# Kernel tuning notes

Measured on AMD Instinct MI355X. Metric: run time of the kernel, lower is better.

The kernel has to match this reference:

```python
import jax, jax.numpy as jnp
import numpy as np

N_NODES = 50000
N_EDGES = 25000
NNZ = 600000
D = 128
H = 256
DEPTH = 2


def setup_inputs() -> dict:
    key = jax.random.key(0)
    ks = jax.random.split(key, 12)
    x = jax.random.normal(ks[0], (N_NODES, D), dtype=jnp.float32)
    v_idx = jax.random.randint(ks[1], (NNZ,), 0, N_NODES)
    e_idx = jax.random.randint(ks[2], (NNZ,), 0, N_EDGES)
    s = 0.05
    W1 = jax.random.normal(ks[3], (H, D), dtype=jnp.float32) * s
    b1 = jnp.zeros((H,), jnp.float32)
    W2 = jax.random.normal(ks[4], (D, H), dtype=jnp.float32) * s
    b2 = jnp.zeros((D,), jnp.float32)
    Wu = jax.random.normal(ks[5], (D, D), dtype=jnp.float32) * s
    bu = jnp.zeros((D,), jnp.float32)
    Wa = jax.random.normal(ks[6], (4, D), dtype=jnp.float32) * s
    ba = jnp.zeros((4,), jnp.float32)
    return {"x": x, "v_idx": v_idx, "e_idx": e_idx, "W1": W1, "b1": b1,
            "W2": W2, "b2": b2, "Wu": Wu, "bu": bu, "Wa": Wa, "ba": ba}


def reference(x, v_idx, e_idx, W1, b1, W2, b2, Wu, bu, Wa, ba):
    ones = jnp.ones((v_idx.shape[0],), x.dtype)
    # degrees for mean aggregation (clamped to avoid div-by-zero)
    edeg = jnp.maximum(jax.ops.segment_sum(ones, e_idx, num_segments=N_EDGES), 1.0)
    vdeg = jnp.maximum(jax.ops.segment_sum(ones, v_idx, num_segments=N_NODES), 1.0)

    def v2v_mean(m):
        # vertex -> hyperedge (mean), then hyperedge -> vertex (mean)
        e_feat = jax.ops.segment_sum(m[v_idx], e_idx, num_segments=N_EDGES) / edeg[:, None]
        return jax.ops.segment_sum(e_feat[e_idx], v_idx, num_segments=N_NODES) / vdeg[:, None]

    def update(h):
        m = jax.nn.relu(h @ W1.T + b1)   # [N, H]
        m = jax.nn.relu(m @ W2.T + b2)   # [N, D]  (dropout = identity in eval)
        m_i = v2v_mean(m)                # [N, D]
        return jax.nn.relu(h @ Wu.T + bu + m_i)

    for _ in range(DEPTH):
        x = update(x)
    a = x @ Wa.T + ba                    # [N, 4]
    return jax.nn.log_softmax(a, axis=1)
```

## Files before the change

### kernel.cpp

```cpp
#include <hip/hip_runtime.h>
#include <hip/hip_bf16.h>
#include <math.h>

#define N_NODES 50000
#define N_EDGES 25000
#define NNZ     600000
#define D       128
#define H       256

#define BW    98
#define NBE   256
#define NBV   511
#define CAPE  3072
#define CAPV  1536
#define CHUNK 4096

typedef short short8 __attribute__((ext_vector_type(8)));
typedef float floatx4 __attribute__((ext_vector_type(4)));

__device__ inline ushort f2bf(float f) {
    uint u = __float_as_uint(f);
    u += 0x7FFF + ((u >> 16) & 1);
    return (ushort)(u >> 16);
}
__device__ inline float bflo(uint u) { return __uint_as_float(u << 16); }
__device__ inline float bfhi(uint u) { return __uint_as_float(u & 0xffff0000u); }

__global__ void convert_and_place(const float* __restrict__ W1, ushort* __restrict__ W1b,
                                  const float* __restrict__ W2, ushort* __restrict__ W2b,
                                  const float* __restrict__ Wu, ushort* __restrict__ Wub,
                                  const int* __restrict__ v_idx, const int* __restrict__ e_idx,
                                  int* __restrict__ cntE, int* __restrict__ cntV,
                                  int2* __restrict__ recE, int2* __restrict__ recV,
                                  int convBlocks) {
    if ((int)blockIdx.x < convBlocks) {
        const int n1 = H * D / 4;
        const int n2 = D * H / 4;
        const int nu = D * D / 4;
        int j = blockIdx.x * 256 + threadIdx.x;
        const float* src; ushort* dst;
        if (j < n1)                { src = W1; dst = W1b; }
        else if ((j -= n1) < n2)   { src = W2; dst = W2b; }
        else if ((j -= n2) < nu)   { src = Wu; dst = Wub; }
        else return;
        float4 v = ((const float4*)src)[j];
        ushort4 o;
        o.x = f2bf(v.x); o.y = f2bf(v.y); o.z = f2bf(v.z); o.w = f2bf(v.w);
        ((ushort4*)dst)[j] = o;
        return;
    }

    __shared__ int hE[NBE], hV[NBV];
    __shared__ int rE[NBE], rV[NBV];
    for (int i = threadIdx.x; i < NBE; i += 256) hE[i] = 0;
    for (int i = threadIdx.x; i < NBV; i += 256) hV[i] = 0;
    __syncthreads();
    int base = (blockIdx.x - convBlocks) * CHUNK;
    int end  = min(base + CHUNK, NNZ);
    int myE[16], myV[16];
    #pragma unroll
    for (int j = 0; j < 16; ++j) {
        int i = base + threadIdx.x + j * 256;
        myE[j] = -1; myV[j] = -1;
        if (i < end) {
            myE[j] = e_idx[i];
            myV[j] = v_idx[i];
            atomicAdd(&hE[myE[j] / BW], 1);
            atomicAdd(&hV[myV[j] / BW], 1);
        }
    }
    __syncthreads();
    for (int i = threadIdx.x; i < NBE; i += 256) {
        int c = hE[i];
        rE[i] = c ? atomicAdd(&cntE[i], c) : 0;
    }
    for (int i = threadIdx.x; i < NBV; i += 256) {
        int c = hV[i];
        rV[i] = c ? atomicAdd(&cntV[i], c) : 0;
    }
    __syncthreads();
    for (int i = threadIdx.x; i < NBE; i += 256) hE[i] = 0;
    for (int i = threadIdx.x; i < NBV; i += 256) hV[i] = 0;
    __syncthreads();
    #pragma unroll
    for (int j = 0; j < 16; ++j) {
        if (myE[j] >= 0) {
            int bk = myE[j] / BW;
            int p = rE[bk] + atomicAdd(&hE[bk], 1);
            recE[(size_t)bk * CAPE + p] = make_int2(myE[j], myV[j]);
            bk = myV[j] / BW;
            p = rV[bk] + atomicAdd(&hV[bk], 1);
            recV[(size_t)bk * CAPV + p] = make_int2(myV[j], myE[j]);
        }
    }
}

__global__ void bucket_final(const int2* __restrict__ recE, const int* __restrict__ cntE,
                             const int2* __restrict__ recV, const int* __restrict__ cntV,
                             int2* __restrict__ e_sd, float* __restrict__ erecip, int* __restrict__ e_vert,
                             int2* __restrict__ v_sd, float* __restrict__ vrecip, int* __restrict__ v_edge) {
    __shared__ int hist[BW], scn[BW], cur[BW];
    const bool eSide = blockIdx.x < NBE;
    const int b = eSide ? blockIdx.x : blockIdx.x - NBE;
    const int cap   = eSide ? CAPE : CAPV;
    const int2* rec = (eSide ? recE : recV) + (size_t)b * cap;
    const int cnt   = (eSide ? cntE : cntV)[b];
    const int nseg  = eSide ? N_EDGES : N_NODES;
    int2* sd        = eSide ? e_sd : v_sd;
    float* recip    = eSide ? erecip : vrecip;
    int* outv       = (eSide ? e_vert : v_edge) + (size_t)b * cap;
    const int k0 = b * BW;

    for (int i = threadIdx.x; i < BW; i += 256) hist[i] = 0;
    __syncthreads();
    for (int i = threadIdx.x; i < cnt; i += 256)
        atomicAdd(&hist[rec[i].x - k0], 1);
    __syncthreads();

    if (threadIdx.x < 64) {
        int lane = threadIdx.x;
        int v0 = hist[lane];
        int a = v0;
        #pragma unroll
        for (int d = 1; d < 64; d <<= 1) {
            int u = __shfl_up(a, d, 64);
            if (lane >= d) a += u;
        }
        scn[lane] = a - v0;
        int tot0 = __shfl(a, 63, 64);
        int v1 = (lane < BW - 64) ? hist[64 + lane] : 0;
        int a1 = v1;
        #pragma unroll
        for (int d = 1; d < 64; d <<= 1) {
            int u = __shfl_up(a1, d, 64);
            if (lane >= d) a1 += u;
        }
        if (lane < BW - 64) scn[64 + lane] = tot0 + a1 - v1;
    }
    __syncthreads();

    const int gbase = b * cap;
    for (int i = threadIdx.x; i < BW; i += 256) {
        int seg = k0 + i;
        if (seg < nseg) {
            sd[seg] = make_int2(gbase + scn[i], hist[i]);
            recip[seg] = 1.0f / (float)max(hist[i], 1);
        }
        cur[i] = scn[i];
    }
    __syncthreads();
    for (int i = threadIdx.x; i < cnt; i += 256) {
        int2 r = rec[i];
        int p = atomicAdd(&cur[r.x - k0], 1);
        outv[p] = r.y;
    }
}

__global__ void gather_rows(const ushort* __restrict__ src,
                            const int2* __restrict__ sd,
                            const int* __restrict__ list,
                            const float* __restrict__ recip,
                            const ushort* __restrict__ uadd,
                            ushort* __restrict__ outbuf,
                            const float* __restrict__ Wa,
                            const float* __restrict__ ba,
                            float* __restrict__ headout,
                            int nseg) {
    long long gtid = (long long)blockIdx.x * blockDim.x + threadIdx.x;
    int seg = (int)(gtid >> 4);
    int ql  = threadIdx.x & 15;
    if (seg >= nseg) return;
    int2 dsc = sd[seg];
    int s = dsc.x, cnt = dsc.y;
    const ushort* sp = src + ql * 8;

    float f0 = 0.f, f1 = 0.f, f2 = 0.f, f3 = 0.f;
    float f4 = 0.f, f5 = 0.f, f6 = 0.f, f7 = 0.f;

    int p = 0;
    for (; p + 4 <= cnt; p += 4) {
        int r0 = list[s + p + 0];
        int r1 = list[s + p + 1];
        int r2 = list[s + p + 2];
        int r3 = list[s + p + 3];
        uint4 t0 = *(const uint4*)(sp + (size_t)r0 * D);
        uint4 t1 = *(const uint4*)(sp + (size_t)r1 * D);
        uint4 t2 = *(const uint4*)(sp + (size_t)r2 * D);
        uint4 t3 = *(const uint4*)(sp + (size_t)r3 * D);
        f0 += bflo(t0.x) + bflo(t1.x) + bflo(t2.x) + bflo(t3.x);
        f1 += bfhi(t0.x) + bfhi(t1.x) + bfhi(t2.x) + bfhi(t3.x);
        f2 += bflo(t0.y) + bflo(t1.y) + bflo(t2.y) + bflo(t3.y);
        f3 += bfhi(t0.y) + bfhi(t1.y) + bfhi(t2.y) + bfhi(t3.y);
        f4 += bflo(t0.z) + bflo(t1.z) + bflo(t2.z) + bflo(t3.z);
        f5 += bfhi(t0.z) + bfhi(t1.z) + bfhi(t2.z) + bfhi(t3.z);
        f6 += bflo(t0.w) + bflo(t1.w) + bflo(t2.w) + bflo(t3.w);
        f7 += bfhi(t0.w) + bfhi(t1.w) + bfhi(t2.w) + bfhi(t3.w);
    }
    for (; p < cnt; ++p) {
        int r0 = list[s + p];
        uint4 t0 = *(const uint4*)(sp + (size_t)r0 * D);
        f0 += bflo(t0.x);  f1 += bfhi(t0.x);
        f2 += bflo(t0.y);  f3 += bfhi(t0.y);
        f4 += bflo(t0.z);  f5 += bfhi(t0.z);
        f6 += bflo(t0.w);  f7 += bfhi(t0.w);
    }

    float rc = recip[seg];
    f0 *= rc; f1 *= rc; f2 *= rc; f3 *= rc;
    f4 *= rc; f5 *= rc; f6 *= rc; f7 *= rc;
    if (uadd) {
        uint4 uv = *(const uint4*)(uadd + (size_t)seg * D + ql * 8);
        f0 = fmaxf(f0 + bflo(uv.x), 0.f);  f1 = fmaxf(f1 + bfhi(uv.x), 0.f);
        f2 = fmaxf(f2 + bflo(uv.y), 0.f);  f3 = fmaxf(f3 + bfhi(uv.y), 0.f);
        f4 = fmaxf(f4 + bflo(uv.z), 0.f);  f5 = fmaxf(f5 + bfhi(uv.z), 0.f);
        f6 = fmaxf(f6 + bflo(uv.w), 0.f);  f7 = fmaxf(f7 + bfhi(uv.w), 0.f);
    }
    if (headout) {
        float av[4];
        #pragma unroll
        for (int j = 0; j < 4; ++j) {
            const float* wr = Wa + j * D + ql * 8;
            float4 wA = *(const float4*)wr;
            float4 wB = *(const float4*)(wr + 4);
            float pj = f0 * wA.x + f1 * wA.y + f2 * wA.z + f3 * wA.w
                     + f4 * wB.x + f5 * wB.y + f6 * wB.z + f7 * wB.w;
            pj += __shfl_xor(pj, 1, 64);
            pj += __shfl_xor(pj, 2, 64);
            pj += __shfl_xor(pj, 4, 64);
            pj += __shfl_xor(pj, 8, 64);
            av[j] = pj + ba[j];
        }
        if (ql == 0) {
            float mx = fmaxf(fmaxf(av[0], av[1]), fmaxf(av[2], av[3]));
            float se = expf(av[0] - mx) + expf(av[1] - mx)
                     + expf(av[2] - mx) + expf(av[3] - mx);
            float lse = mx + logf(se);
            float4 o = make_float4(av[0] - lse, av[1] - lse, av[2] - lse, av[3] - lse);
            *(float4*)(headout + (size_t)seg * 4) = o;
        }
    } else {
        uint4 o;
        o.x = ((uint)f2bf(f1) << 16) | (uint)f2bf(f0);
        o.y = ((uint)f2bf(f3) << 16) | (uint)f2bf(f2);
        o.z = ((uint)f2bf(f5) << 16) | (uint)f2bf(f4);
        o.w = ((uint)f2bf(f7) << 16) | (uint)f2bf(f6);
        *(uint4*)(outbuf + (size_t)seg * D + ql * 8) = o;
    }
}

__launch_bounds__(256, 2)
__global__ void mlp_fused(const void* __restrict__ Aptr, int a_fp32,
                          const ushort* __restrict__ W1b,
                          const float* __restrict__ b1,
                          const ushort* __restrict__ W2b,
                          const float* __restrict__ b2,
                          const ushort* __restrict__ Wub,
                          const float* __restrict__ bu,
                          ushort* __restrict__ m2out,
                          ushort* __restrict__ uout,
                          int M) {
    __shared__ ushort Af[128][136];
    __shared__ __align__(16) char Pbuf[18432];
    __shared__ ushort m1c[128][72];
    ushort* P = (ushort*)Pbuf;

    const int tid = threadIdx.x;
    const int w = tid >> 6, lane = tid & 63;
    const int quad = lane >> 4, mrow = lane & 15;
    const int rowBase = blockIdx.x * 128;

    #pragma unroll
    for (int r = 0; r < 8; ++r) {
        int idx = tid + r * 256;
        int row = idx >> 4;
        int c   = (idx & 15) << 3;
        uint4 av = make_uint4(0, 0, 0, 0);
        if (rowBase + row < M) {
            if (a_fp32) {
                const float* ap = (const float*)Aptr + (size_t)(rowBase + row) * D + c;
                float4 va = *(const float4*)ap;
                float4 vb = *(const float4*)(ap + 4);
                av.x = ((uint)f2bf(va.y) << 16) | (uint)f2bf(va.x);
                av.y = ((uint)f2bf(va.w) << 16) | (uint)f2bf(va.z);
                av.z = ((uint)f2bf(vb.y) << 16) | (uint)f2bf(vb.x);
                av.w = ((uint)f2bf(vb.w) << 16) | (uint)f2bf(vb.z);
            } else {
                av = *(const uint4*)((const ushort*)Aptr + (size_t)(rowBase + row) * D + c);
            }
        }
        *(uint4*)&Af[row][c] = av;
    }

    for (int n0 = 0; n0 < D; n0 += 64) {
        __syncthreads();
        #pragma unroll
        for (int r = 0; r < 4; ++r) {
            int idx = tid + r * 256;
            int row = idx >> 4;
            int c   = (idx & 15) << 3;
            *(uint4*)&P[row * 136 + c] = *(const uint4*)(Wub + (size_t)(n0 + row) * D + c);
        }
        __syncthreads();
        #pragma unroll
        for (int rg = 0; rg < 2; ++rg) {
            floatx4 acc[4] = {{0,0,0,0},{0,0,0,0},{0,0,0,0},{0,0,0,0}};
            #pragma unroll
            for (int k0 = 0; k0 < D; k0 += 32) {
                short8 af = *(const short8*)&Af[rg * 64 + w * 16 + mrow][k0 + quad * 8];
                #pragma unroll
                for (int t = 0; t < 4; ++t) {
                    short8 bfr = *(const short8*)&P[(t * 16 + mrow) * 136 + k0 + quad * 8];
                    acc[t] = __builtin_amdgcn_mfma_f32_16x16x32_bf16(af, bfr, acc[t], 0, 0, 0);
                }
            }
            int growb = rowBase + rg * 64 + w * 16 + quad * 4;
            if (growb < M) {
                #pragma unroll
                for (int t = 0; t < 4; ++t) {
                    float bb = bu[n0 + t * 16 + mrow];
                    #pragma unroll
                    for (int r = 0; r < 4; ++r)
                        uout[(size_t)(growb + r) * D + n0 + t * 16 + mrow] =
                            f2bf(acc[t][r] + bb);
                }
            }
        }
    }

    floatx4 acc2[2][8] = {};
    for (int kc = 0; kc < 4; ++kc) {
        __syncthreads();
        #pragma unroll
        for (int r = 0; r < 4; ++r) {
            int idx = tid + r * 256;
            int row = idx >> 4;
            int c   = (idx & 15) << 3;
            *(uint4*)&P[row * 136 + c] = *(const uint4*)(W1b + (size_t)(kc * 64 + row) * D + c);
        }
        __syncthreads();
        #pragma unroll
        for (int rg = 0; rg < 2; ++rg) {
            floatx4 acc1[4] = {{0,0,0,0},{0,0,0,0},{0,0,0,0},{0,0,0,0}};
            #pragma unroll
            for (int k0 = 0; k0 < D; k0 += 32) {
                short8 af = *(const short8*)&Af[rg * 64 + w * 16 + mrow][k0 + quad * 8];
                #pragma unroll
                for (int t = 0; t < 4; ++t) {
                    short8 bfr = *(const short8*)&P[(t * 16 + mrow) * 136 + k0 + quad * 8];
                    acc1[t] = __builtin_amdgcn_mfma_f32_16x16x32_bf16(af, bfr, acc1[t], 0, 0, 0);
                }
            }
            #pragma unroll
            for (int t = 0; t < 4; ++t) {
                float bb = b1[kc * 64 + t * 16 + mrow];
                #pragma unroll
                for (int r = 0; r < 4; ++r)
                    m1c[rg * 64 + w * 16 + quad * 4 + r][t * 16 + mrow] =
                        f2bf(fmaxf(acc1[t][r] + bb, 0.f));
            }
        }
        __syncthreads();
        #pragma unroll
        for (int r = 0; r < 4; ++r) {
            int idx = tid + r * 256;
            int row = idx >> 3;
            int c8  = (idx & 7) << 3;
            *(uint4*)&P[row * 72 + c8] = *(const uint4*)(W2b + (size_t)row * H + kc * 64 + c8);
        }
        __syncthreads();
        #pragma unroll
        for (int rg = 0; rg < 2; ++rg) {
            #pragma unroll
            for (int k0 = 0; k0 < 64; k0 += 32) {
                short8 af = *(const short8*)&m1c[rg * 64 + w * 16 + mrow][k0 + quad * 8];
                #pragma unroll
                for (int t2 = 0; t2 < 8; ++t2) {
                    short8 bfr = *(const short8*)&P[(t2 * 16 + mrow) * 72 + k0 + quad * 8];
                    acc2[rg][t2] = __builtin_amdgcn_mfma_f32_16x16x32_bf16(af, bfr, acc2[rg][t2], 0, 0, 0);
                }
            }
        }
    }

    #pragma unroll
    for (int rg = 0; rg < 2; ++rg) {
        int growb = rowBase + rg * 64 + w * 16 + quad * 4;
        if (growb < M) {
            #pragma unroll
            for (int t2 = 0; t2 < 8; ++t2) {
                float bb = b2[t2 * 16 + mrow];
                #pragma unroll
                for (int r = 0; r < 4; ++r)
                    m2out[(size_t)(growb + r) * D + t2 * 16 + mrow] =
                        f2bf(fmaxf(acc2[rg][t2][r] + bb, 0.f));
            }
        }
    }
}

extern "C" void kernel_launch(void* const* d_in, const int* in_sizes, int n_in,
                              void* d_out, int out_size, void* d_ws, size_t ws_size,
                              hipStream_t stream) {
    const float* x     = (const float*)d_in[0];
    const int*   v_idx = (const int*)d_in[1];
    const int*   e_idx = (const int*)d_in[2];
    const float* W1    = (const float*)d_in[3];
    const float* b1    = (const float*)d_in[4];
    const float* W2    = (const float*)d_in[5];
    const float* b2    = (const float*)d_in[6];
    const float* Wu    = (const float*)d_in[7];
    const float* bu    = (const float*)d_in[8];
    const float* Wa    = (const float*)d_in[9];
    const float* ba    = (const float*)d_in[10];
    float* out = (float*)d_out;

    char* wsp = (char*)d_ws;
    auto alloc = [&](size_t bytes) -> char* {
        char* p = wsp;
        wsp += (bytes + 255) & ~(size_t)255;
        return p;
    };

    ushort* hA     = (ushort*)alloc((size_t)N_NODES * D * 2);
    ushort* m2b    = (ushort*)alloc((size_t)N_NODES * D * 2);
    ushort* ub     = (ushort*)alloc((size_t)N_NODES * D * 2);
    ushort* e_feat = (ushort*)alloc((size_t)N_EDGES * D * 2);
    ushort* W1b    = (ushort*)alloc((size_t)H * D * 2);
    ushort* W2b    = (ushort*)alloc((size_t)D * H * 2);
    ushort* Wub    = (ushort*)alloc((size_t)D * D * 2);
    int*    e_vert = (int*)alloc((size_t)NBE * CAPE * 4);
    int*    v_edge = (int*)alloc((size_t)NBV * CAPV * 4);
    int2*   recE   = (int2*)alloc((size_t)NBE * CAPE * 8);
    int2*   recV   = (int2*)alloc((size_t)NBV * CAPV * 8);
    int*    cntE   = (int*)alloc((size_t)(NBE + NBV) * 4);
    int*    cntV   = cntE + NBE;
    int2*   e_sd   = (int2*)alloc((size_t)N_EDGES * 8);
    int2*   v_sd   = (int2*)alloc((size_t)N_NODES * 8);
    float*  erecip = (float*)alloc((size_t)N_EDGES * 4);
    float*  vrecip = (float*)alloc((size_t)N_NODES * 4);

    const int cooBlocks  = (NNZ + CHUNK - 1) / CHUNK;
    const int convTotal  = H * D / 4 + D * H / 4 + D * D / 4;
    const int convBlocks = (convTotal + 255) / 256;

    hipMemsetAsync(cntE, 0, (size_t)(NBE + NBV) * 4, stream);
    convert_and_place<<<convBlocks + cooBlocks, 256, 0, stream>>>(
        W1, W1b, W2, W2b, Wu, Wub, v_idx, e_idx, cntE, cntV, recE, recV, convBlocks);
    bucket_final<<<NBE + NBV, 256, 0, stream>>>(recE, cntE, recV, cntV,
                                                e_sd, erecip, e_vert,
                                                v_sd, vrecip, v_edge);

    const int gridM = (N_NODES + 127) / 128;
    const int gEdge = (N_EDGES * 16 + 255) / 256;
    const int gVert = (N_NODES * 16 + 255) / 256;

    const void* h = x;
    int h_fp32 = 1;
    for (int depth = 0; depth < 2; ++depth) {
        mlp_fused<<<gridM, 256, 0, stream>>>(h, h_fp32, W1b, b1, W2b, b2, Wub, bu,
                                             m2b, ub, N_NODES);
        gather_rows<<<gEdge, 256, 0, stream>>>(
            m2b, e_sd, e_vert, erecip, nullptr, e_feat, nullptr, nullptr, nullptr, N_EDGES);
        if (depth == 0) {
            gather_rows<<<gVert, 256, 0, stream>>>(
                e_feat, v_sd, v_edge, vrecip, ub, hA, nullptr, nullptr, nullptr, N_NODES);
            h = hA;
            h_fp32 = 0;
        } else {
            gather_rows<<<gVert, 256, 0, stream>>>(
                e_feat, v_sd, v_edge, vrecip, ub, nullptr, Wa, ba, out, N_NODES);
        }
    }
}
```

Before: 253.4 us.

## Use 512-thread MLP blocks with one row-group per wave; unroll gather by 8

```diff
diff --git a/kernel.cpp b/kernel.cpp
--- a/kernel.cpp
+++ b/kernel.cpp
@@ -178,6 +178,40 @@
     float f4 = 0.f, f5 = 0.f, f6 = 0.f, f7 = 0.f;
 
     int p = 0;
+    for (; p + 8 <= cnt; p += 8) {
+        int r0 = list[s + p + 0];
+        int r1 = list[s + p + 1];
+        int r2 = list[s + p + 2];
+        int r3 = list[s + p + 3];
+        int r4 = list[s + p + 4];
+        int r5 = list[s + p + 5];
+        int r6 = list[s + p + 6];
+        int r7 = list[s + p + 7];
+        uint4 t0 = *(const uint4*)(sp + (size_t)r0 * D);
+        uint4 t1 = *(const uint4*)(sp + (size_t)r1 * D);
+        uint4 t2 = *(const uint4*)(sp + (size_t)r2 * D);
+        uint4 t3 = *(const uint4*)(sp + (size_t)r3 * D);
+        uint4 t4 = *(const uint4*)(sp + (size_t)r4 * D);
+        uint4 t5 = *(const uint4*)(sp + (size_t)r5 * D);
+        uint4 t6 = *(const uint4*)(sp + (size_t)r6 * D);
+        uint4 t7 = *(const uint4*)(sp + (size_t)r7 * D);
+        f0 += bflo(t0.x)+bflo(t1.x)+bflo(t2.x)+bflo(t3.x)
+            + bflo(t4.x)+bflo(t5.x)+bflo(t6.x)+bflo(t7.x);
+        f1 += bfhi(t0.x)+bfhi(t1.x)+bfhi(t2.x)+bfhi(t3.x)
+            + bfhi(t4.x)+bfhi(t5.x)+bfhi(t6.x)+bfhi(t7.x);
+        f2 += bflo(t0.y)+bflo(t1.y)+bflo(t2.y)+bflo(t3.y)
+            + bflo(t4.y)+bflo(t5.y)+bflo(t6.y)+bflo(t7.y);
+        f3 += bfhi(t0.y)+bfhi(t1.y)+bfhi(t2.y)+bfhi(t3.y)
+            + bfhi(t4.y)+bfhi(t5.y)+bfhi(t6.y)+bfhi(t7.y);
+        f4 += bflo(t0.z)+bflo(t1.z)+bflo(t2.z)+bflo(t3.z)
+            + bflo(t4.z)+bflo(t5.z)+bflo(t6.z)+bflo(t7.z);
+        f5 += bfhi(t0.z)+bfhi(t1.z)+bfhi(t2.z)+bfhi(t3.z)
+            + bfhi(t4.z)+bfhi(t5.z)+bfhi(t6.z)+bfhi(t7.z);
+        f6 += bflo(t0.w)+bflo(t1.w)+bflo(t2.w)+bflo(t3.w)
+            + bflo(t4.w)+bflo(t5.w)+bflo(t6.w)+bflo(t7.w);
+        f7 += bfhi(t0.w)+bfhi(t1.w)+bfhi(t2.w)+bfhi(t3.w)
+            + bfhi(t4.w)+bfhi(t5.w)+bfhi(t6.w)+bfhi(t7.w);
+    }
     for (; p + 4 <= cnt; p += 4) {
         int r0 = list[s + p + 0];
         int r1 = list[s + p + 1];
@@ -248,7 +282,7 @@
     }
 }
 
-__launch_bounds__(256, 2)
+__launch_bounds__(512, 4)
 __global__ void mlp_fused(const void* __restrict__ Aptr, int a_fp32,
                           const ushort* __restrict__ W1b,
                           const float* __restrict__ b1,
@@ -265,13 +299,15 @@
     ushort* P = (ushort*)Pbuf;
 
     const int tid = threadIdx.x;
-    const int w = tid >> 6, lane = tid & 63;
+    const int w = tid >> 6;
+    const int lane = tid & 63;
     const int quad = lane >> 4, mrow = lane & 15;
     const int rowBase = blockIdx.x * 128;
+    const int wr0 = w * 16;
 
     #pragma unroll
-    for (int r = 0; r < 8; ++r) {
-        int idx = tid + r * 256;
+    for (int r = 0; r < 4; ++r) {
+        int idx = tid + r * 512;
         int row = idx >> 4;
         int c   = (idx & 15) << 3;
         uint4 av = make_uint4(0, 0, 0, 0);
@@ -294,97 +330,87 @@
     for (int n0 = 0; n0 < D; n0 += 64) {
         __syncthreads();
         #pragma unroll
-        for (int r = 0; r < 4; ++r) {
-            int idx = tid + r * 256;
+        for (int r = 0; r < 2; ++r) {
+            int idx = tid + r * 512;
             int row = idx >> 4;
             int c   = (idx & 15) << 3;
             *(uint4*)&P[row * 136 + c] = *(const uint4*)(Wub + (size_t)(n0 + row) * D + c);
         }
         __syncthreads();
-        #pragma unroll
-        for (int rg = 0; rg < 2; ++rg) {
-            floatx4 acc[4] = {{0,0,0,0},{0,0,0,0},{0,0,0,0},{0,0,0,0}};
+        floatx4 acc[4] = {{0,0,0,0},{0,0,0,0},{0,0,0,0},{0,0,0,0}};
+        #pragma unroll
+        for (int k0 = 0; k0 < D; k0 += 32) {
+            short8 af = *(const short8*)&Af[wr0 + mrow][k0 + quad * 8];
             #pragma unroll
-            for (int k0 = 0; k0 < D; k0 += 32) {
-                short8 af = *(const short8*)&Af[rg * 64 + w * 16 + mrow][k0 + quad * 8];
+            for (int t = 0; t < 4; ++t) {
+                short8 bfr = *(const short8*)&P[(t * 16 + mrow) * 136 + k0 + quad * 8];
+                acc[t] = __builtin_amdgcn_mfma_f32_16x16x32_bf16(af, bfr, acc[t], 0, 0, 0);
+            }
+        }
+        int growb = rowBase + wr0 + quad * 4;
+        if (growb < M) {
+            #pragma unroll
+            for (int t = 0; t < 4; ++t) {
+                float bb = bu[n0 + t * 16 + mrow];
                 #pragma unroll
-                for (int t = 0; t < 4; ++t) {
-                    short8 bfr = *(const short8*)&P[(t * 16 + mrow) * 136 + k0 + quad * 8];
-                    acc[t] = __builtin_amdgcn_mfma_f32_16x16x32_bf16(af, bfr, acc[t], 0, 0, 0);
-                }
+                for (int r = 0; r < 4; ++r)
+                    uout[(size_t)(growb + r) * D + n0 + t * 16 + mrow] =
+                        f2bf(acc[t][r] + bb);
             }
-            int growb = rowBase + rg * 64 + w * 16 + quad * 4;
-            if (growb < M) {
-                #pragma unroll
-                for (int t = 0; t < 4; ++t) {
-                    float bb = bu[n0 + t * 16 + mrow];
-                    #pragma unroll
-                    for (int r = 0; r < 4; ++r)
-                        uout[(size_t)(growb + r) * D + n0 + t * 16 + mrow] =
-                            f2bf(acc[t][r] + bb);
-                }
-            }
-        }
-    }
-
-    floatx4 acc2[2][8] = {};
+        }
+    }
+
+    floatx4 acc2[8] = {};
     for (int kc = 0; kc < 4; ++kc) {
         __syncthreads();
         #pragma unroll
-        for (int r = 0; r < 4; ++r) {
-            int idx = tid + r * 256;
+        for (int r = 0; r < 2; ++r) {
+            int idx = tid + r * 512;
             int row = idx >> 4;
             int c   = (idx & 15) << 3;
             *(uint4*)&P[row * 136 + c] = *(const uint4*)(W1b + (size_t)(kc * 64 + row) * D + c);
         }
         __syncthreads();
-        #pragma unroll
-        for (int rg = 0; rg < 2; ++rg) {
-            floatx4 acc1[4] = {{0,0,0,0},{0,0,0,0},{0,0,0,0},{0,0,0,0}};
-            #pragma unroll
-            for (int k0 = 0; k0 < D; k0 += 32) {
-                short8 af = *(const short8*)&Af[rg * 64 + w * 16 + mrow][k0 + quad * 8];
-                #pragma unroll
-                for (int t = 0; t < 4; ++t) {
-                    short8 bfr = *(const short8*)&P[(t * 16 + mrow) * 136 + k0 + quad * 8];
-                    acc1[t] = __builtin_amdgcn_mfma_f32_16x16x32_bf16(af, bfr, acc1[t], 0, 0, 0);
-                }
-            }
+        floatx4 acc1[4] = {{0,0,0,0},{0,0,0,0},{0,0,0,0},{0,0,0,0}};
+        #pragma unroll
+        for (int k0 = 0; k0 < D; k0 += 32) {
+            short8 af = *(const short8*)&Af[wr0 + mrow][k0 + quad * 8];
             #pragma unroll
             for (int t = 0; t < 4; ++t) {
-                float bb = b1[kc * 64 + t * 16 + mrow];
-                #pragma unroll
-                for (int r = 0; r < 4; ++r)
-                    m1c[rg * 64 + w * 16 + quad * 4 + r][t * 16 + mrow] =
-                        f2bf(fmaxf(acc1[t][r] + bb, 0.f));
+                short8 bfr = *(const short8*)&P[(t * 16 + mrow) * 136 + k0 + quad * 8];
+                acc1[t] = __builtin_amdgcn_mfma_f32_16x16x32_bf16(af, bfr, acc1[t], 0, 0, 0);
             }
         }
+        #pragma unroll
+        for (int t = 0; t < 4; ++t) {
+            float bb = b1[kc * 64 + t * 16 + mrow];
+            #pragma unroll
+            for (int r = 0; r < 4; ++r)
+                m1c[wr0 + quad * 4 + r][t * 16 + mrow] =
+                    f2bf(fmaxf(acc1[t][r] + bb, 0.f));
+        }
         __syncthreads();
         #pragma unroll
-        for (int r = 0; r < 4; ++r) {
-            int idx = tid + r * 256;
+        for (int r = 0; r < 2; ++r) {
+            int idx = tid + r * 512;
             int row = idx >> 3;
             int c8  = (idx & 7) << 3;
             *(uint4*)&P[row * 72 + c8] = *(const uint4*)(W2b + (size_t)row * H + kc * 64 + c8);
         }
         __syncthreads();
         #pragma unroll
-        for (int rg = 0; rg < 2; ++rg) {
+        for (int k0 = 0; k0 < 64; k0 += 32) {
+            short8 af = *(const short8*)&m1c[wr0 + mrow][k0 + quad * 8];
             #pragma unroll
-            for (int k0 = 0; k0 < 64; k0 += 32) {
-                short8 af = *(const short8*)&m1c[rg * 64 + w * 16 + mrow][k0 + quad * 8];
-                #pragma unroll
-                for (int t2 = 0; t2 < 8; ++t2) {
-                    short8 bfr = *(const short8*)&P[(t2 * 16 + mrow) * 72 + k0 + quad * 8];
-                    acc2[rg][t2] = __builtin_amdgcn_mfma_f32_16x16x32_bf16(af, bfr, acc2[rg][t2], 0, 0, 0);
-                }
+            for (int t2 = 0; t2 < 8; ++t2) {
+                short8 bfr = *(const short8*)&P[(t2 * 16 + mrow) * 72 + k0 + quad * 8];
+                acc2[t2] = __builtin_amdgcn_mfma_f32_16x16x32_bf16(af, bfr, acc2[t2], 0, 0, 0);
             }
         }
     }
 
-    #pragma unroll
-    for (int rg = 0; rg < 2; ++rg) {
-        int growb = rowBase + rg * 64 + w * 16 + quad * 4;
+    {
+        int growb = rowBase + wr0 + quad * 4;
         if (growb < M) {
             #pragma unroll
             for (int t2 = 0; t2 < 8; ++t2) {
@@ -392,7 +418,7 @@
                 #pragma unroll
                 for (int r = 0; r < 4; ++r)
                     m2out[(size_t)(growb + r) * D + t2 * 16 + mrow] =
-                        f2bf(fmaxf(acc2[rg][t2][r] + bb, 0.f));
+                        f2bf(fmaxf(acc2[t2][r] + bb, 0.f));
             }
         }
     }
@@ -457,7 +483,7 @@
     const void* h = x;
     int h_fp32 = 1;
     for (int depth = 0; depth < 2; ++depth) {
-        mlp_fused<<<gridM, 256, 0, stream>>>(h, h_fp32, W1b, b1, W2b, b2, Wub, bu,
+        mlp_fused<<<gridM, 512, 0, stream>>>(h, h_fp32, W1b, b1, W2b, b2, Wub, bu,
                                              m2b, ub, N_NODES);
         gather_rows<<<gEdge, 256, 0, stream>>>(
             m2b, e_sd, e_vert, erecip, nullptr, e_feat, nullptr, nullptr, nullptr, N_EDGES);
```

Result: slower. 260.2 us (+2.7%).
